# Performance work log

Hardware: AMD Instinct MI355X
Metric: run time of the kernel (lower is better)

Reference implementation:

```python
import jax, jax.numpy as jnp
import numpy as np

B, D_IN, R, D_P, K, D_C, ITERS = 4096, 2048, 7, 128, 25, 16, 3


def _ln(x, g, b, eps=1e-5):
    m = jnp.mean(x, axis=-1, keepdims=True)
    v = jnp.var(x, axis=-1, keepdims=True)
    return (x - m) * jax.lax.rsqrt(v + eps) * g + b


def _squash(x):
    eps = 1e-6
    ns = jnp.sum(x * x, axis=-1, keepdims=True)
    scale = ns / jnp.maximum(1.0 + ns, eps)
    return scale * x / (jnp.sqrt(ns) + eps)


def setup_inputs() -> dict:
    key = jax.random.key(0)
    ks = jax.random.split(key, 8)
    f = lambda k, shp, s=0.02: (jax.random.normal(k, shp) * s).astype(jnp.float32)
    return {
        "z": jax.random.normal(ks[0], (B, D_IN), jnp.float32),
        "W_prim": f(ks[1], (D_IN, R * D_P)),
        "b_prim": jnp.zeros((R * D_P,), jnp.float32),
        "ln_a_g": jnp.ones((D_IN,), jnp.float32),
        "ln_a_b": jnp.zeros((D_IN,), jnp.float32),
        "W_act": f(ks[2], (D_IN, R)),
        "b_act": jnp.zeros((R,), jnp.float32),
        "w_caps": (np.sqrt(K / (D_P * R)).astype(np.float32)
                   * jax.random.normal(ks[3], (R, D_P, K, D_C))).astype(jnp.float32),
        "ln_c_g": jnp.ones((D_C,), jnp.float32),
        "ln_c_b": jnp.zeros((D_C,), jnp.float32),
        "beta_u": f(ks[4], (K,), 1.0),
        "ln_h_g": jnp.ones((R * D_C,), jnp.float32),
        "ln_h_b": jnp.zeros((R * D_C,), jnp.float32),
        "W_h1": f(ks[5], (R * D_C, 4 * R * D_C)),
        "b_h1": jnp.zeros((4 * R * D_C,), jnp.float32),
        "W_h2": f(ks[6], (4 * R * D_C, 1)),
        "b_h2": jnp.zeros((1,), jnp.float32),
    }


def reference(z, W_prim, b_prim, ln_a_g, ln_a_b, W_act, b_act, w_caps,
              ln_c_g, ln_c_b, beta_u, ln_h_g, ln_h_b, W_h1, b_h1, W_h2, b_h2):
    # primary capsules: [B, R, D_P] poses + [B, R] activations
    pose = _squash((z @ W_prim + b_prim).reshape(B, R, D_P))
    act = jnp.clip(jax.nn.sigmoid(_ln(z, ln_a_g, ln_a_b) @ W_act + b_act), 0.0, 1.0)

    # votes: [B, R, K, D_C]
    u = jnp.einsum('brd,rdkh->brkh', pose, w_caps)
    scale = 1.0 / np.sqrt(D_C).astype(np.float32)

    # iterative routing (EM/softmax-agreement style)
    q = jnp.full((B, R, K), 1.0 / K, dtype=z.dtype)
    class_pose = None
    for _ in range(ITERS):
        wts = q * act[:, :, None]                               # [B,R,K]
        class_pose = _ln(jnp.einsum('brk,brkh->bkh', wts, u), ln_c_g, ln_c_b)
        agree = jnp.einsum('bkh,brkh->brk', class_pose, u) * scale
        q = jax.nn.softmax(agree, axis=-1)

    class_act = jax.nn.sigmoid(beta_u[None, :] + jnp.einsum('brk,br->bk', q, act))
    route_class_emb = q[..., None] * u                          # [B,R,K,D_C]

    # concat per-route interaction vectors -> [B, K, R*D_C]
    class_embed = jnp.transpose(route_class_emb, (0, 2, 1, 3)).reshape(B, K, R * D_C)
    h = jax.nn.gelu(_ln(class_embed, ln_h_g, ln_h_b) @ W_h1 + b_h1, approximate=False)
    logits = (h @ W_h2 + b_h2)[..., 0]                          # [B, K]

    return (logits, class_embed, class_pose, class_act, q, pose, act, route_class_emb)
```

## Files before the change

kernel.cpp:

```cpp
#include <hip/hip_runtime.h>
#include <cstddef>

#define BB 4096
#define DIN 2048
#define RR 7
#define DP 128
#define KK 25
#define DC 16
#define NITERS 3
#define RKH (RR*KK*DC)
#define RK  (RR*KK)
#define KH  (KK*DC)
#define HD  (RR*DC)
#define H4  (4*HD)

typedef __attribute__((ext_vector_type(8))) short bf16x8;
typedef __attribute__((ext_vector_type(4))) float f32x4;

__device__ __forceinline__ unsigned pk_bf16(float a, float b) {
    union { float f; unsigned u; } xa, xb;
    xa.f = a; xb.f = b;
    unsigned ua = (xa.u + 0x7FFFu + ((xa.u >> 16) & 1u)) >> 16;
    unsigned ub = (xb.u + 0x7FFFu + ((xb.u >> 16) & 1u)) >> 16;
    return (ua & 0xFFFFu) | (ub << 16);
}

__device__ __forceinline__ float gelu_tanh(float x) {
    float x3 = x * x * x;
    float tt = 0.7978845608f * (x + 0.044715f * x3);
    float e = __expf(2.0f * tt);
    float th = 1.0f - 2.0f / (e + 1.0f);
    return 0.5f * x * (1.0f + th);
}

__global__ __launch_bounds__(256) void transpose_cvt_kernel(
    const float* __restrict__ src, unsigned short* __restrict__ dst, int RS, int CS)
{
    __shared__ float T[64][65];
    int r0 = blockIdx.x * 64, c0 = blockIdx.y * 64;
    size_t bo = (size_t)blockIdx.z * RS * CS;
    src += bo; dst += bo;
    int t = threadIdx.x;
    for (int s = t; s < 64 * 16; s += 256) {
        int row = s >> 4, c4 = s & 15;
        int gr = r0 + row, gc = c0 + c4 * 4;
        float4 v = make_float4(0.f, 0.f, 0.f, 0.f);
        if (gr < RS && gc < CS) v = *(const float4*)(src + (size_t)gr * CS + gc);
        T[row][c4 * 4 + 0] = v.x; T[row][c4 * 4 + 1] = v.y;
        T[row][c4 * 4 + 2] = v.z; T[row][c4 * 4 + 3] = v.w;
    }
    __syncthreads();
    for (int s = t; s < 64 * 16; s += 256) {
        int col = s >> 4, r4 = s & 15;
        int gc = c0 + col, gr = r0 + r4 * 4;
        if (gc < CS && gr + 3 < RS) {
            unsigned lo = pk_bf16(T[r4 * 4 + 0][col], T[r4 * 4 + 1][col]);
            unsigned hi = pk_bf16(T[r4 * 4 + 2][col], T[r4 * 4 + 3][col]);
            *(uint2*)(dst + (size_t)gc * RS + gr) = make_uint2(lo, hi);
        }
    }
}

__global__ __launch_bounds__(256) void w1_frag_kernel(
    const float* __restrict__ W1, unsigned short* __restrict__ W1F)
{
    int d = blockIdx.x * 256 + threadIdx.x;
    int e2 = d & 3;
    int lane = (d >> 2) & 63;
    int fid = d >> 8;
    int j = fid & 3, ks = (fid >> 2) & 3, nc = fid >> 4;
    int col = nc * 64 + j * 16 + (lane & 15);
    int k = ks * 32 + (lane >> 4) * 8 + e2 * 2;
    float a = (k < HD)     ? W1[(size_t)k * H4 + col]       : 0.f;
    float b = (k + 1 < HD) ? W1[(size_t)(k + 1) * H4 + col] : 0.f;
    ((unsigned*)W1F)[d] = pk_bf16(a, b);
}

__global__ __launch_bounds__(256) void act_kernel(
    const float* __restrict__ z, const float* __restrict__ g, const float* __restrict__ bb,
    const float* __restrict__ Wa, const float* __restrict__ ba,
    float* __restrict__ act_out)
{
    int b = blockIdx.x;
    int t = threadIdx.x;
    __shared__ float zs[DIN];
    __shared__ float ws1[4], ws2[4];
    __shared__ float wr[4][RR];
    const float* zr = z + (size_t)b * DIN;
    float s = 0.f, s2 = 0.f;
    for (int i = t; i < DIN; i += 256) {
        float v = zr[i]; zs[i] = v; s += v; s2 += v * v;
    }
    for (int off = 32; off; off >>= 1) { s += __shfl_down(s, off); s2 += __shfl_down(s2, off); }
    int w = t >> 6, lane = t & 63;
    if (lane == 0) { ws1[w] = s; ws2[w] = s2; }
    __syncthreads();
    s  = ws1[0] + ws1[1] + ws1[2] + ws1[3];
    s2 = ws2[0] + ws2[1] + ws2[2] + ws2[3];
    float mean = s * (1.0f / DIN);
    float var  = s2 * (1.0f / DIN) - mean * mean;
    float rstd = rsqrtf(var + 1e-5f);
    float acc[RR];
#pragma unroll
    for (int r = 0; r < RR; ++r) acc[r] = 0.f;
    for (int i = t; i < DIN; i += 256) {
        float y = (zs[i] - mean) * rstd * g[i] + bb[i];
#pragma unroll
        for (int r = 0; r < RR; ++r) acc[r] += y * Wa[i * RR + r];
    }
    for (int off = 32; off; off >>= 1) {
#pragma unroll
        for (int r = 0; r < RR; ++r) acc[r] += __shfl_down(acc[r], off);
    }
    if (lane == 0) {
#pragma unroll
        for (int r = 0; r < RR; ++r) wr[w][r] = acc[r];
    }
    __syncthreads();
    if (t < RR) {
        float v = wr[0][t] + wr[1][t] + wr[2][t] + wr[3][t] + ba[t];
        float sg = 1.0f / (1.0f + expf(-v));
        sg = fminf(fmaxf(sg, 0.0f), 1.0f);
        act_out[(size_t)b * RR + t] = sg;
    }
}

__global__ __launch_bounds__(256) void pose_mfma(
    const float* __restrict__ z, const unsigned short* __restrict__ WpT,
    const float* __restrict__ bp, float* __restrict__ pose_out)
{
    __shared__ __align__(16) unsigned short As[128 * 40];
    __shared__ __align__(16) unsigned short Bs[128 * 40];
    __shared__ float sq[2][128];
    int m0 = blockIdx.x * 128, r = blockIdx.y, t = threadIdx.x;
    int n0 = r * DP;
    int w = t >> 6, l = t & 63;
    int lrow = l & 15, koff = l >> 4;
    int rbase = (w >> 1) * 64, cbase = (w & 1) * 64;
    f32x4 acc[4][4];
#pragma unroll
    for (int i = 0; i < 4; ++i)
#pragma unroll
        for (int j = 0; j < 4; ++j) acc[i][j] = 0.0f;
    for (int kt = 0; kt < DIN; kt += 32) {
#pragma unroll
        for (int q = 0; q < 4; ++q) {
            int s = t + 256 * q;
            int row = s >> 3, k4 = s & 7;
            float4 v = *(const float4*)(z + (size_t)(m0 + row) * DIN + kt + k4 * 4);
            *(uint2*)(As + row * 40 + k4 * 4) = make_uint2(pk_bf16(v.x, v.y), pk_bf16(v.z, v.w));
        }
#pragma unroll
        for (int q = 0; q < 2; ++q) {
            int s = t + 256 * q;
            int col = s >> 2, k8 = s & 3;
            uint4 v = *(const uint4*)(WpT + (size_t)(n0 + col) * DIN + kt + k8 * 8);
            *(uint4*)(Bs + col * 40 + k8 * 8) = v;
        }
        __syncthreads();
        bf16x8 a[4], b[4];
#pragma unroll
        for (int i = 0; i < 4; ++i)
            a[i] = *(const bf16x8*)(As + (rbase + i * 16 + lrow) * 40 + koff * 8);
#pragma unroll
        for (int j = 0; j < 4; ++j)
            b[j] = *(const bf16x8*)(Bs + (cbase + j * 16 + lrow) * 40 + koff * 8);
#pragma unroll
        for (int i = 0; i < 4; ++i)
#pragma unroll
            for (int j = 0; j < 4; ++j)
                acc[i][j] = __builtin_amdgcn_mfma_f32_16x16x32_bf16(a[i], b[j], acc[i][j], 0, 0, 0);
        __syncthreads();
    }
    float bpv[4];
#pragma unroll
    for (int j = 0; j < 4; ++j) bpv[j] = bp[n0 + cbase + j * 16 + lrow];
    float ns_[4][4];
#pragma unroll
    for (int i = 0; i < 4; ++i)
#pragma unroll
        for (int reg = 0; reg < 4; ++reg) {
            float ss = 0.f;
#pragma unroll
            for (int j = 0; j < 4; ++j) {
                float x = acc[i][j][reg] + bpv[j];
                acc[i][j][reg] = x;
                ss += x * x;
            }
            ss += __shfl_xor(ss, 1); ss += __shfl_xor(ss, 2);
            ss += __shfl_xor(ss, 4); ss += __shfl_xor(ss, 8);
            ns_[i][reg] = ss;
        }
    if (lrow == 0) {
#pragma unroll
        for (int i = 0; i < 4; ++i)
#pragma unroll
            for (int reg = 0; reg < 4; ++reg)
                sq[w & 1][rbase + i * 16 + koff * 4 + reg] = ns_[i][reg];
    }
    __syncthreads();
#pragma unroll
    for (int i = 0; i < 4; ++i)
#pragma unroll
        for (int reg = 0; reg < 4; ++reg) {
            int rl = rbase + i * 16 + koff * 4 + reg;
            float ns = sq[0][rl] + sq[1][rl];
            float factor = (ns / fmaxf(1.0f + ns, 1e-6f)) / (sqrtf(ns) + 1e-6f);
            size_t rowbase = ((size_t)(m0 + rl) * RR + r) * DP;
#pragma unroll
            for (int j = 0; j < 4; ++j)
                pose_out[rowbase + cbase + j * 16 + lrow] = acc[i][j][reg] * factor;
        }
}

__global__ __launch_bounds__(256) void votes_mfma(
    const float* __restrict__ pose, const unsigned short* __restrict__ wcT,
    float* __restrict__ u_out)
{
    __shared__ __align__(16) unsigned short As[128 * 152];
    __shared__ __align__(16) unsigned short Bs[80 * 152];
    int m0 = blockIdx.x * 128, r = blockIdx.y, n0 = blockIdx.z * 80;
    int t = threadIdx.x;
    int w = t >> 6, l = t & 63;
    int lrow = l & 15, koff = l >> 4;
    int rbase = w * 32;
#pragma unroll
    for (int q = 0; q < 16; ++q) {
        int s = t + 256 * q;
        int row = s >> 5, k4 = s & 31;
        float4 v = *(const float4*)(pose + ((size_t)(m0 + row) * RR + r) * DP + k4 * 4);
        *(uint2*)(As + row * 152 + k4 * 4) = make_uint2(pk_bf16(v.x, v.y), pk_bf16(v.z, v.w));
    }
    const unsigned short* wr_ = wcT + (size_t)r * KH * DP;
#pragma unroll
    for (int q = 0; q < 5; ++q) {
        int s = t + 256 * q;
        int col = s >> 4, k8 = s & 15;
        uint4 v = *(const uint4*)(wr_ + (size_t)(n0 + col) * DP + k8 * 8);
        *(uint4*)(Bs + col * 152 + k8 * 8) = v;
    }
    __syncthreads();
    f32x4 acc[2][5];
#pragma unroll
    for (int i = 0; i < 2; ++i)
#pragma unroll
        for (int j = 0; j < 5; ++j) acc[i][j] = 0.0f;
#pragma unroll
    for (int ks = 0; ks < 4; ++ks) {
        bf16x8 a[2], b[5];
#pragma unroll
        for (int i = 0; i < 2; ++i)
            a[i] = *(const bf16x8*)(As + (rbase + i * 16 + lrow) * 152 + ks * 32 + koff * 8);
#pragma unroll
        for (int j = 0; j < 5; ++j)
            b[j] = *(const bf16x8*)(Bs + (j * 16 + lrow) * 152 + ks * 32 + koff * 8);
#pragma unroll
        for (int i = 0; i < 2; ++i)
#pragma unroll
            for (int j = 0; j < 5; ++j)
                acc[i][j] = __builtin_amdgcn_mfma_f32_16x16x32_bf16(a[i], b[j], acc[i][j], 0, 0, 0);
    }
#pragma unroll
    for (int i = 0; i < 2; ++i)
#pragma unroll
        for (int reg = 0; reg < 4; ++reg) {
            int row = m0 + rbase + i * 16 + koff * 4 + reg;
            size_t base = ((size_t)row * RR + r) * KH + n0;
#pragma unroll
            for (int j = 0; j < 5; ++j)
                u_out[base + j * 16 + lrow] = acc[i][j][reg];
        }
}

__global__ __launch_bounds__(64) void routing_kernel(
    const float* __restrict__ u_in, const float* __restrict__ act_in,
    const float* __restrict__ lncg, const float* __restrict__ lncb,
    const float* __restrict__ beta_u,
    float* __restrict__ q_out, float* __restrict__ cp_out,
    float* __restrict__ ca_out, float* __restrict__ rce_out,
    float* __restrict__ ce_out)
{
    __shared__ __align__(16) float U[RKH];
    __shared__ float Q[RK];
    __shared__ float CP[KH];
    __shared__ float AG[RK];
    __shared__ float A7[RR];
    int b = blockIdx.x, t = threadIdx.x;
    const float4* u4 = (const float4*)(u_in + (size_t)b * RKH);
    float4* U4 = (float4*)U;
    for (int p = t; p < RKH / 4; p += 64) U4[p] = u4[p];
    if (t < RR) A7[t] = act_in[(size_t)b * RR + t];
    for (int p = t; p < RK; p += 64) Q[p] = 1.0f / KK;
    __syncthreads();
    for (int it = 0; it < NITERS; ++it) {
        for (int p = t; p < KH; p += 64) {
            int k = p / DC;
            float s = 0.f;
#pragma unroll
            for (int r = 0; r < RR; ++r) s += Q[r * KK + k] * A7[r] * U[r * KH + p];
            CP[p] = s;
        }
        __syncthreads();
        if (t < KK) {
            float m = 0.f;
#pragma unroll
            for (int h = 0; h < DC; ++h) m += CP[t * DC + h];
            m *= (1.0f / DC);
            float v = 0.f;
#pragma unroll
            for (int h = 0; h < DC; ++h) { float d = CP[t * DC + h] - m; v += d * d; }
            v *= (1.0f / DC);
            float rstd = rsqrtf(v + 1e-5f);
#pragma unroll
            for (int h = 0; h < DC; ++h)
                CP[t * DC + h] = (CP[t * DC + h] - m) * rstd * lncg[h] + lncb[h];
        }
        __syncthreads();
        for (int p = t; p < RK; p += 64) {
            int r = p / KK, k = p % KK;
            float s = 0.f;
#pragma unroll
            for (int h = 0; h < DC; ++h) s += CP[k * DC + h] * U[r * KH + k * DC + h];
            AG[p] = s * 0.25f;
        }
        __syncthreads();
        if (t < RR) {
            float mx = -1e30f;
            for (int k = 0; k < KK; ++k) mx = fmaxf(mx, AG[t * KK + k]);
            float e[KK], sum = 0.f;
            for (int k = 0; k < KK; ++k) { e[k] = expf(AG[t * KK + k] - mx); sum += e[k]; }
            float inv = 1.0f / sum;
            for (int k = 0; k < KK; ++k) Q[t * KK + k] = e[k] * inv;
        }
        __syncthreads();
    }
    if (t < KK) {
        float s = 0.f;
#pragma unroll
        for (int r = 0; r < RR; ++r) s += Q[r * KK + t] * A7[r];
        ca_out[(size_t)b * KK + t] = 1.0f / (1.0f + expf(-(beta_u[t] + s)));
    }
    for (int p = t; p < RK; p += 64) q_out[(size_t)b * RK + p] = Q[p];
    for (int p = t; p < KH; p += 64) cp_out[(size_t)b * KH + p] = CP[p];
    float4* rce4 = (float4*)(rce_out + (size_t)b * RKH);
    float4* ce4  = (float4*)ce_out;
    for (int p4 = t; p4 < RKH / 4; p4 += 64) {
        int base = p4 * 4;
        int r  = base / KH;
        int k  = (base % KH) / DC;
        int h0 = base % DC;
        float qv = Q[r * KK + k];
        float4 uv = U4[p4];
        float4 rv = make_float4(qv * uv.x, qv * uv.y, qv * uv.z, qv * uv.w);
        rce4[p4] = rv;
        size_t ci = ((size_t)b * RKH + (size_t)k * HD + (size_t)r * DC + h0) >> 2;
        ce4[ci] = rv;
    }
}

__global__ __launch_bounds__(256) void head_mfma(
    const float* __restrict__ ce, const float* __restrict__ g, const float* __restrict__ bb,
    const unsigned short* __restrict__ W1F, const float* __restrict__ b1,
    const float* __restrict__ W2, const float* __restrict__ b2,
    float* __restrict__ logits)
{
    __shared__ __align__(16) unsigned short As[128 * 128];
    __shared__ __align__(16) unsigned short Bs[448 * 128];
    __shared__ float LB1[H4];
    __shared__ float LW2[H4];
    int row0 = blockIdx.x * 128;
    int t = threadIdx.x;
    int w = t >> 6, l = t & 63;
    int lrow = l & 15, koff = l >> 4;

#pragma unroll
    for (int q = 0; q < 28; ++q) {
        int chunk = w * 28 + q;
        __builtin_amdgcn_global_load_lds(
            (const __attribute__((address_space(1))) unsigned int*)(const void*)(W1F + (size_t)chunk * 512 + l * 8),
            (__attribute__((address_space(3))) unsigned int*)(void*)(Bs + chunk * 512),
            16, 0, 0);
    }
    for (int s = t; s < H4; s += 256) { LB1[s] = b1[s]; LW2[s] = W2[s]; }

    {
        int row = t >> 1, half = t & 1;
        const float* rp = ce + (size_t)(row0 + row) * HD + half * 56;
        float4 v[14];
#pragma unroll
        for (int m = 0; m < 14; ++m) v[m] = *(const float4*)(rp + m * 4);
        float s1 = 0.f, s2 = 0.f;
#pragma unroll
        for (int m = 0; m < 14; ++m) {
            s1 += v[m].x + v[m].y + v[m].z + v[m].w;
            s2 += v[m].x * v[m].x + v[m].y * v[m].y + v[m].z * v[m].z + v[m].w * v[m].w;
        }
        s1 += __shfl_xor(s1, 1); s2 += __shfl_xor(s2, 1);
        float mean = s1 * (1.0f / HD);
        float var  = s2 * (1.0f / HD) - mean * mean;
        float rstd = rsqrtf(var + 1e-5f);
        int lr = row & 15, rt = row >> 4;
#pragma unroll
        for (int j = 0; j < 7; ++j) {
            float4 gl0 = *(const float4*)(g  + half * 56 + j * 8);
            float4 gl1 = *(const float4*)(g  + half * 56 + j * 8 + 4);
            float4 bl0 = *(const float4*)(bb + half * 56 + j * 8);
            float4 bl1 = *(const float4*)(bb + half * 56 + j * 8 + 4);
            float4 x0 = v[j * 2], x1 = v[j * 2 + 1];
            float y0 = (x0.x - mean) * rstd * gl0.x + bl0.x;
            float y1 = (x0.y - mean) * rstd * gl0.y + bl0.y;
            float y2 = (x0.z - mean) * rstd * gl0.z + bl0.z;
            float y3 = (x0.w - mean) * rstd * gl0.w + bl0.w;
            float y4 = (x1.x - mean) * rstd * gl1.x + bl1.x;
            float y5 = (x1.y - mean) * rstd * gl1.y + bl1.y;
            float y6 = (x1.z - mean) * rstd * gl1.z + bl1.z;
            float y7 = (x1.w - mean) * rstd * gl1.w + bl1.w;
            int k8 = half * 7 + j;
            int ks = k8 >> 2, ko = k8 & 3;
            unsigned* dst = (unsigned*)(As + (size_t)((rt * 4 + ks) * 64 + ko * 16 + lr) * 8);
            dst[0] = pk_bf16(y0, y1); dst[1] = pk_bf16(y2, y3);
            dst[2] = pk_bf16(y4, y5); dst[3] = pk_bf16(y6, y7);
        }
        if (half) {
            uint4 z4 = make_uint4(0, 0, 0, 0);
            *(uint4*)(As + (size_t)((rt * 4 + 3) * 64 + 2 * 16 + lr) * 8) = z4;
            *(uint4*)(As + (size_t)((rt * 4 + 3) * 64 + 3 * 16 + lr) * 8) = z4;
        }
    }
    __syncthreads();

    bf16x8 af[2][4];
#pragma unroll
    for (int i = 0; i < 2; ++i)
#pragma unroll
        for (int ks = 0; ks < 4; ++ks)
            af[i][ks] = *(const bf16x8*)(As + (size_t)(((w * 2 + i) * 4 + ks) * 64 + l) * 8);

    float logitAcc[2][4];
#pragma unroll
    for (int i = 0; i < 2; ++i)
#pragma unroll
        for (int reg = 0; reg < 4; ++reg) logitAcc[i][reg] = 0.f;

    for (int nc = 0; nc < 7; ++nc) {
        float b1v[4], w2v[4];
#pragma unroll
        for (int j = 0; j < 4; ++j) {
            b1v[j] = LB1[nc * 64 + j * 16 + lrow];
            w2v[j] = LW2[nc * 64 + j * 16 + lrow];
        }
        f32x4 acc[2][4];
#pragma unroll
        for (int i = 0; i < 2; ++i)
#pragma unroll
            for (int j = 0; j < 4; ++j) acc[i][j] = 0.0f;
#pragma unroll
        for (int ks = 0; ks < 4; ++ks) {
            bf16x8 b[4];
#pragma unroll
            for (int j = 0; j < 4; ++j)
                b[j] = *(const bf16x8*)(Bs + (size_t)(((nc * 4 + ks) * 4 + j) * 64 + l) * 8);
#pragma unroll
            for (int i = 0; i < 2; ++i)
#pragma unroll
                for (int j = 0; j < 4; ++j)
                    acc[i][j] = __builtin_amdgcn_mfma_f32_16x16x32_bf16(af[i][ks], b[j], acc[i][j], 0, 0, 0);
        }
#pragma unroll
        for (int i = 0; i < 2; ++i)
#pragma unroll
            for (int reg = 0; reg < 4; ++reg) {
                float sum = 0.f;
#pragma unroll
                for (int j = 0; j < 4; ++j) {
                    float x = acc[i][j][reg] + b1v[j];
                    sum += gelu_tanh(x) * w2v[j];
                }
                logitAcc[i][reg] += sum;
            }
    }
#pragma unroll
    for (int i = 0; i < 2; ++i)
#pragma unroll
        for (int reg = 0; reg < 4; ++reg) {
            float vv = logitAcc[i][reg];
            vv += __shfl_xor(vv, 1); vv += __shfl_xor(vv, 2);
            vv += __shfl_xor(vv, 4); vv += __shfl_xor(vv, 8);
            logitAcc[i][reg] = vv;
        }
    if (lrow == 0) {
        float b2v = b2[0];
#pragma unroll
        for (int i = 0; i < 2; ++i)
#pragma unroll
            for (int reg = 0; reg < 4; ++reg)
                logits[row0 + w * 32 + i * 16 + koff * 4 + reg] = logitAcc[i][reg] + b2v;
    }
}

__global__ __launch_bounds__(256) void pose_kernel(
    const float* __restrict__ z, const float* __restrict__ Wp, const float* __restrict__ bp,
    float* __restrict__ pose_out)
{
    __shared__ __align__(16) float As[64 * 36];
    __shared__ __align__(16) float Bs[32 * 128];
    int m0 = blockIdx.x * 64;
    int r  = blockIdx.y;
    int n0 = r * DP;
    int t  = threadIdx.x;
    int rg = t >> 5;
    int cg = t & 31;
    float acc[8][4] = {};
    for (int kt = 0; kt < DIN; kt += 32) {
#pragma unroll
        for (int q = 0; q < 2; ++q) {
            int s = t * 2 + q;
            int row = s >> 3, k4 = s & 7;
            float4 v = *(const float4*)(z + (size_t)(m0 + row) * DIN + kt + k4 * 4);
            *(float4*)(As + row * 36 + k4 * 4) = v;
        }
#pragma unroll
        for (int q = 0; q < 4; ++q) {
            int s = t + 256 * q;
            int row = s >> 5, c4 = s & 31;
            float4 v = *(const float4*)(Wp + (size_t)(kt + row) * (RR * DP) + n0 + c4 * 4);
            *(float4*)(Bs + row * 128 + c4 * 4) = v;
        }
        __syncthreads();
#pragma unroll
        for (int kk = 0; kk < 32; ++kk) {
            float4 bv = *(const float4*)(Bs + kk * 128 + cg * 4);
#pragma unroll
            for (int j = 0; j < 8; ++j) {
                float a = As[(rg * 8 + j) * 36 + kk];
                acc[j][0] += a * bv.x; acc[j][1] += a * bv.y;
                acc[j][2] += a * bv.z; acc[j][3] += a * bv.w;
            }
        }
        __syncthreads();
    }
    float bi0 = bp[n0 + cg * 4], bi1 = bp[n0 + cg * 4 + 1];
    float bi2 = bp[n0 + cg * 4 + 2], bi3 = bp[n0 + cg * 4 + 3];
#pragma unroll
    for (int j = 0; j < 8; ++j) {
        float x0 = acc[j][0] + bi0, x1 = acc[j][1] + bi1;
        float x2 = acc[j][2] + bi2, x3 = acc[j][3] + bi3;
        float ns = x0 * x0 + x1 * x1 + x2 * x2 + x3 * x3;
        for (int off = 1; off < 32; off <<= 1) ns += __shfl_xor(ns, off);
        float factor = (ns / fmaxf(1.0f + ns, 1e-6f)) / (sqrtf(ns) + 1e-6f);
        int row = m0 + rg * 8 + j;
        float4 o = make_float4(x0 * factor, x1 * factor, x2 * factor, x3 * factor);
        *(float4*)(pose_out + ((size_t)row * RR + r) * DP + cg * 4) = o;
    }
}

__global__ __launch_bounds__(256) void votes_kernel(
    const float* __restrict__ pose, const float* __restrict__ wc,
    float* __restrict__ u_out)
{
    __shared__ float As[64 * 129];
    __shared__ __align__(16) float Bs[64 * 80];
    int m0 = blockIdx.x * 64;
    int r  = blockIdx.y;
    int n0 = blockIdx.z * 80;
    int t  = threadIdx.x;
    const size_t wbase = (size_t)r * DP * KH;
#pragma unroll
    for (int q = 0; q < 8; ++q) {
        int s = t + 256 * q;
        int row = s >> 5, d4 = s & 31;
        float4 v = *(const float4*)(pose + ((size_t)(m0 + row) * RR + r) * DP + d4 * 4);
        As[row * 129 + d4 * 4 + 0] = v.x;
        As[row * 129 + d4 * 4 + 1] = v.y;
        As[row * 129 + d4 * 4 + 2] = v.z;
        As[row * 129 + d4 * 4 + 3] = v.w;
    }
    int m4 = t >> 4, n5 = t & 15;
    float acc[4][5];
#pragma unroll
    for (int i = 0; i < 4; ++i)
#pragma unroll
        for (int j = 0; j < 5; ++j) acc[i][j] = 0.f;
    for (int kt = 0; kt < DP; kt += 64) {
        __syncthreads();
#pragma unroll
        for (int q = 0; q < 5; ++q) {
            int s = t + 256 * q;
            int d = s / 20, c4 = s % 20;
            float4 v = *(const float4*)(wc + wbase + (size_t)(kt + d) * KH + n0 + c4 * 4);
            *(float4*)(Bs + d * 80 + c4 * 4) = v;
        }
        __syncthreads();
#pragma unroll 4
        for (int dd = 0; dd < 64; ++dd) {
            int d = kt + dd;
            float b_[5];
#pragma unroll
            for (int j = 0; j < 5; ++j) b_[j] = Bs[dd * 80 + n5 * 5 + j];
#pragma unroll
            for (int i = 0; i < 4; ++i) {
                float a = As[(m4 * 4 + i) * 129 + d];
#pragma unroll
                for (int j = 0; j < 5; ++j) acc[i][j] += a * b_[j];
            }
        }
    }
#pragma unroll
    for (int i = 0; i < 4; ++i) {
        int row = m0 + m4 * 4 + i;
        size_t base = ((size_t)row * RR + r) * KH + n0 + n5 * 5;
#pragma unroll
        for (int j = 0; j < 5; ++j) u_out[base + j] = acc[i][j];
    }
}

__global__ __launch_bounds__(256) void head_kernel(
    const float* __restrict__ ce, const float* __restrict__ g, const float* __restrict__ bb,
    const float* __restrict__ W1, const float* __restrict__ b1,
    const float* __restrict__ W2, const float* __restrict__ b2,
    float* __restrict__ logits)
{
    __shared__ __align__(16) float Y[64 * HD];
    __shared__ float Wc[HD * 64];
    __shared__ float Lg[64];
    int row0 = blockIdx.x * 64;
    int t = threadIdx.x;
    for (int s = t; s < 64 * HD; s += 256) Y[s] = ce[(size_t)row0 * HD + s];
    __syncthreads();
    if (t < 64) {
        float m = 0.f;
        for (int i = 0; i < HD; ++i) m += Y[t * HD + i];
        m *= (1.0f / HD);
        float v = 0.f;
        for (int i = 0; i < HD; ++i) { float d = Y[t * HD + i] - m; v += d * d; }
        v *= (1.0f / HD);
        float rstd = rsqrtf(v + 1e-5f);
        for (int i = 0; i < HD; ++i) Y[t * HD + i] = (Y[t * HD + i] - m) * rstd * g[i] + bb[i];
    }
    int rg = t >> 4;
    int cg = t & 15;
    float accRow[4] = {0.f, 0.f, 0.f, 0.f};
    for (int c0 = 0; c0 < H4; c0 += 64) {
        __syncthreads();
        for (int s = t; s < HD * 64; s += 256) {
            int i = s >> 6, c = s & 63;
            Wc[i * 64 + c] = W1[(size_t)i * H4 + c0 + c];
        }
        __syncthreads();
        float b1v[4], w2v[4];
#pragma unroll
        for (int c = 0; c < 4; ++c) { b1v[c] = b1[c0 + cg * 4 + c]; w2v[c] = W2[c0 + cg * 4 + c]; }
        float s_[4][4];
#pragma unroll
        for (int rr = 0; rr < 4; ++rr)
#pragma unroll
            for (int c = 0; c < 4; ++c) s_[rr][c] = b1v[c];
        for (int i4 = 0; i4 < HD / 4; ++i4) {
            float4 y4[4];
#pragma unroll
            for (int rr = 0; rr < 4; ++rr)
                y4[rr] = *(const float4*)(Y + (rg * 4 + rr) * HD + i4 * 4);
#pragma unroll
            for (int is = 0; is < 4; ++is) {
                float w_[4];
#pragma unroll
                for (int c = 0; c < 4; ++c) w_[c] = Wc[(i4 * 4 + is) * 64 + cg * 4 + c];
#pragma unroll
                for (int rr = 0; rr < 4; ++rr) {
                    float yv = (is == 0) ? y4[rr].x : (is == 1) ? y4[rr].y : (is == 2) ? y4[rr].z : y4[rr].w;
#pragma unroll
                    for (int c = 0; c < 4; ++c) s_[rr][c] += yv * w_[c];
                }
            }
        }
#pragma unroll
        for (int rr = 0; rr < 4; ++rr) {
#pragma unroll
            for (int c = 0; c < 4; ++c) {
                float x = s_[rr][c];
                float ge = 0.5f * x * (1.0f + erff(x * 0.70710678118654752440f));
                accRow[rr] += ge * w2v[c];
            }
        }
    }
#pragma unroll
    for (int rr = 0; rr < 4; ++rr) {
        float v = accRow[rr];
        v += __shfl_xor(v, 1); v += __shfl_xor(v, 2);
        v += __shfl_xor(v, 4); v += __shfl_xor(v, 8);
        if (cg == 0) Lg[rg * 4 + rr] = v;
    }
    __syncthreads();
    if (t < 64) logits[row0 + t] = Lg[t] + b2[0];
}

extern "C" void kernel_launch(void* const* d_in, const int* in_sizes, int n_in,
                              void* d_out, int out_size, void* d_ws, size_t ws_size,
                              hipStream_t stream) {
    const float* z    = (const float*)d_in[0];
    const float* Wp   = (const float*)d_in[1];
    const float* bp   = (const float*)d_in[2];
    const float* lnag = (const float*)d_in[3];
    const float* lnab = (const float*)d_in[4];
    const float* Wa   = (const float*)d_in[5];
    const float* ba   = (const float*)d_in[6];
    const float* wc   = (const float*)d_in[7];
    const float* lncg = (const float*)d_in[8];
    const float* lncb = (const float*)d_in[9];
    const float* beta = (const float*)d_in[10];
    const float* lnhg = (const float*)d_in[11];
    const float* lnhb = (const float*)d_in[12];
    const float* W1   = (const float*)d_in[13];
    const float* b1   = (const float*)d_in[14];
    const float* W2   = (const float*)d_in[15];
    const float* b2   = (const float*)d_in[16];

    float* out = (float*)d_out;
    float* o_logits = out;
    float* o_ce   = o_logits + (size_t)BB * KK;
    float* o_cp   = o_ce   + (size_t)BB * KK * HD;
    float* o_ca   = o_cp   + (size_t)BB * KK * DC;
    float* o_q    = o_ca   + (size_t)BB * KK;
    float* o_pose = o_q    + (size_t)BB * RK;
    float* o_act  = o_pose + (size_t)BB * RR * DP;
    float* o_rce  = o_act  + (size_t)BB * RR;

    const size_t WPT_ELE = (size_t)(RR * DP) * DIN;
    const size_t W1F_ELE = (size_t)H4 * 128;
    const size_t WCT_ELE = (size_t)RR * KH * DP;
    const size_t WS_NEED = (WPT_ELE + W1F_ELE + WCT_ELE) * sizeof(unsigned short);
    unsigned short* WpT = (unsigned short*)d_ws;
    unsigned short* W1F = WpT + WPT_ELE;
    unsigned short* wcT = W1F + W1F_ELE;

    hipLaunchKernelGGL(act_kernel, dim3(BB), dim3(256), 0, stream,
                       z, lnag, lnab, Wa, ba, o_act);

    if (ws_size >= WS_NEED) {
        hipLaunchKernelGGL(transpose_cvt_kernel, dim3(DIN / 64, (RR * DP) / 64, 1), dim3(256), 0, stream,
                           Wp, WpT, DIN, RR * DP);
        hipLaunchKernelGGL(w1_frag_kernel, dim3(112), dim3(256), 0, stream,
                           W1, W1F);
        hipLaunchKernelGGL(transpose_cvt_kernel, dim3(2, 7, RR), dim3(256), 0, stream,
                           wc, wcT, DP, KH);
        hipLaunchKernelGGL(pose_mfma, dim3(BB / 128, RR), dim3(256), 0, stream,
                           z, WpT, bp, o_pose);
        hipLaunchKernelGGL(votes_mfma, dim3(BB / 128, RR, 5), dim3(256), 0, stream,
                           o_pose, wcT, o_rce);
        hipLaunchKernelGGL(routing_kernel, dim3(BB), dim3(64), 0, stream,
                           o_rce, o_act, lncg, lncb, beta, o_q, o_cp, o_ca, o_rce, o_ce);
        hipLaunchKernelGGL(head_mfma, dim3(BB * KK / 128), dim3(256), 0, stream,
                           o_ce, lnhg, lnhb, W1F, b1, W2, b2, o_logits);
    } else {
        hipLaunchKernelGGL(pose_kernel, dim3(BB / 64, RR), dim3(256), 0, stream,
                           z, Wp, bp, o_pose);
        hipLaunchKernelGGL(votes_kernel, dim3(BB / 64, RR, 5), dim3(256), 0, stream,
                           o_pose, wc, o_rce);
        hipLaunchKernelGGL(routing_kernel, dim3(BB), dim3(64), 0, stream,
                           o_rce, o_act, lncg, lncb, beta, o_q, o_cp, o_ca, o_rce, o_ce);
        hipLaunchKernelGGL(head_kernel, dim3(BB * KK / 64), dim3(256), 0, stream,
                           o_ce, lnhg, lnhb, W1, b1, W2, b2, o_logits);
    }
}
```

Baseline: 382.6 us.

## Make head kernel persistent with 512 threads, prefetch next tile, cheaper GELU

The head MLP kernel becomes persistent: 256 blocks of 512 threads loop over the 800 row tiles. Each block loads the bf16 W1 fragments into LDS once instead of once per tile. While the MFMAs for the current tile run, half the threads prefetch the next tile's class-embedding rows into registers. Each wave now computes 16 rows instead of 32, and the tanh-form GELU is rewritten as a sigmoid form using a fast reciprocal. The cost is more synchronisation per tile, less per-wave MFMA reuse of each B fragment, and a slightly different approximation of GELU.

```diff
diff --git a/kernel.cpp b/kernel.cpp
--- a/kernel.cpp
+++ b/kernel.cpp
@@ -13,6 +13,7 @@
 #define KH  (KK*DC)
 #define HD  (RR*DC)
 #define H4  (4*HD)
+#define HEAD_TILES (BB*KK/128)
 
 typedef __attribute__((ext_vector_type(8))) short bf16x8;
 typedef __attribute__((ext_vector_type(4))) float f32x4;
@@ -31,6 +32,13 @@
     float e = __expf(2.0f * tt);
     float th = 1.0f - 2.0f / (e + 1.0f);
     return 0.5f * x * (1.0f + th);
+}
+
+__device__ __forceinline__ float gelu_fast(float x) {
+    float u = x * __builtin_fmaf(x * x, 0.07135655f, 1.5957691f);
+    u = fmaxf(u, -30.0f);
+    float e = __expf(-u);
+    return x * __builtin_amdgcn_rcpf(1.0f + e);
 }
 
 __global__ __launch_bounds__(256) void transpose_cvt_kernel(
@@ -358,7 +366,7 @@
     }
 }
 
-__global__ __launch_bounds__(256) void head_mfma(
+__global__ __launch_bounds__(512) void head_mfma(
     const float* __restrict__ ce, const float* __restrict__ g, const float* __restrict__ bb,
     const unsigned short* __restrict__ W1F, const float* __restrict__ b1,
     const float* __restrict__ W2, const float* __restrict__ b2,
@@ -368,133 +376,133 @@
     __shared__ __align__(16) unsigned short Bs[448 * 128];
     __shared__ float LB1[H4];
     __shared__ float LW2[H4];
-    int row0 = blockIdx.x * 128;
     int t = threadIdx.x;
     int w = t >> 6, l = t & 63;
     int lrow = l & 15, koff = l >> 4;
 
 #pragma unroll
-    for (int q = 0; q < 28; ++q) {
-        int chunk = w * 28 + q;
+    for (int q = 0; q < 14; ++q) {
+        int chunk = w * 14 + q;
         __builtin_amdgcn_global_load_lds(
             (const __attribute__((address_space(1))) unsigned int*)(const void*)(W1F + (size_t)chunk * 512 + l * 8),
             (__attribute__((address_space(3))) unsigned int*)(void*)(Bs + chunk * 512),
             16, 0, 0);
     }
-    for (int s = t; s < H4; s += 256) { LB1[s] = b1[s]; LW2[s] = W2[s]; }
-
-    {
-        int row = t >> 1, half = t & 1;
-        const float* rp = ce + (size_t)(row0 + row) * HD + half * 56;
-        float4 v[14];
+    if (t >= 256) {
+        for (int s = t - 256; s < H4; s += 256) { LB1[s] = b1[s]; LW2[s] = W2[s]; }
+    }
+    float b2v = b2[0];
+
+    int row = t >> 1, half = t & 1;
+    int lr = row & 15, rt = row >> 4;
+
+    float4 v[14];
+    int tile = blockIdx.x;
+    if (t < 256 && tile < HEAD_TILES) {
+        const float* rp = ce + (size_t)(tile * 128 + row) * HD + half * 56;
 #pragma unroll
         for (int m = 0; m < 14; ++m) v[m] = *(const float4*)(rp + m * 4);
-        float s1 = 0.f, s2 = 0.f;
-#pragma unroll
-        for (int m = 0; m < 14; ++m) {
-            s1 += v[m].x + v[m].y + v[m].z + v[m].w;
-            s2 += v[m].x * v[m].x + v[m].y * v[m].y + v[m].z * v[m].z + v[m].w * v[m].w;
-        }
-        s1 += __shfl_xor(s1, 1); s2 += __shfl_xor(s2, 1);
-        float mean = s1 * (1.0f / HD);
-        float var  = s2 * (1.0f / HD) - mean * mean;
-        float rstd = rsqrtf(var + 1e-5f);
-        int lr = row & 15, rt = row >> 4;
-#pragma unroll
-        for (int j = 0; j < 7; ++j) {
-            float4 gl0 = *(const float4*)(g  + half * 56 + j * 8);
-            float4 gl1 = *(const float4*)(g  + half * 56 + j * 8 + 4);
-            float4 bl0 = *(const float4*)(bb + half * 56 + j * 8);
-            float4 bl1 = *(const float4*)(bb + half * 56 + j * 8 + 4);
-            float4 x0 = v[j * 2], x1 = v[j * 2 + 1];
-            float y0 = (x0.x - mean) * rstd * gl0.x + bl0.x;
-            float y1 = (x0.y - mean) * rstd * gl0.y + bl0.y;
-            float y2 = (x0.z - mean) * rstd * gl0.z + bl0.z;
-            float y3 = (x0.w - mean) * rstd * gl0.w + bl0.w;
-            float y4 = (x1.x - mean) * rstd * gl1.x + bl1.x;
-            float y5 = (x1.y - mean) * rstd * gl1.y + bl1.y;
-            float y6 = (x1.z - mean) * rstd * gl1.z + bl1.z;
-            float y7 = (x1.w - mean) * rstd * gl1.w + bl1.w;
-            int k8 = half * 7 + j;
-            int ks = k8 >> 2, ko = k8 & 3;
-            unsigned* dst = (unsigned*)(As + (size_t)((rt * 4 + ks) * 64 + ko * 16 + lr) * 8);
-            dst[0] = pk_bf16(y0, y1); dst[1] = pk_bf16(y2, y3);
-            dst[2] = pk_bf16(y4, y5); dst[3] = pk_bf16(y6, y7);
-        }
-        if (half) {
-            uint4 z4 = make_uint4(0, 0, 0, 0);
-            *(uint4*)(As + (size_t)((rt * 4 + 3) * 64 + 2 * 16 + lr) * 8) = z4;
-            *(uint4*)(As + (size_t)((rt * 4 + 3) * 64 + 3 * 16 + lr) * 8) = z4;
-        }
-    }
-    __syncthreads();
-
-    bf16x8 af[2][4];
-#pragma unroll
-    for (int i = 0; i < 2; ++i)
+    }
+
+    bool first = true;
+    for (; tile < HEAD_TILES; tile += 256) {
+        if (!first) __syncthreads();
+        first = false;
+
+        if (t < 256) {
+            float s1 = 0.f, s2 = 0.f;
+#pragma unroll
+            for (int m = 0; m < 14; ++m) {
+                s1 += v[m].x + v[m].y + v[m].z + v[m].w;
+                s2 += v[m].x * v[m].x + v[m].y * v[m].y + v[m].z * v[m].z + v[m].w * v[m].w;
+            }
+            s1 += __shfl_xor(s1, 1); s2 += __shfl_xor(s2, 1);
+            float mean = s1 * (1.0f / HD);
+            float var  = s2 * (1.0f / HD) - mean * mean;
+            float rstd = rsqrtf(var + 1e-5f);
+#pragma unroll
+            for (int j = 0; j < 7; ++j) {
+                float4 gl0 = *(const float4*)(g  + half * 56 + j * 8);
+                float4 gl1 = *(const float4*)(g  + half * 56 + j * 8 + 4);
+                float4 bl0 = *(const float4*)(bb + half * 56 + j * 8);
+                float4 bl1 = *(const float4*)(bb + half * 56 + j * 8 + 4);
+                float4 x0 = v[j * 2], x1 = v[j * 2 + 1];
+                float y0 = (x0.x - mean) * rstd * gl0.x + bl0.x;
+                float y1 = (x0.y - mean) * rstd * gl0.y + bl0.y;
+                float y2 = (x0.z - mean) * rstd * gl0.z + bl0.z;
+                float y3 = (x0.w - mean) * rstd * gl0.w + bl0.w;
+                float y4 = (x1.x - mean) * rstd * gl1.x + bl1.x;
+                float y5 = (x1.y - mean) * rstd * gl1.y + bl1.y;
+                float y6 = (x1.z - mean) * rstd * gl1.z + bl1.z;
+                float y7 = (x1.w - mean) * rstd * gl1.w + bl1.w;
+                int k8 = half * 7 + j;
+                int ks = k8 >> 2, ko = k8 & 3;
+                unsigned* dst = (unsigned*)(As + (size_t)((rt * 4 + ks) * 64 + ko * 16 + lr) * 8);
+                dst[0] = pk_bf16(y0, y1); dst[1] = pk_bf16(y2, y3);
+                dst[2] = pk_bf16(y4, y5); dst[3] = pk_bf16(y6, y7);
+            }
+            if (half) {
+                uint4 z4 = make_uint4(0, 0, 0, 0);
+                *(uint4*)(As + (size_t)((rt * 4 + 3) * 64 + 2 * 16 + lr) * 8) = z4;
+                *(uint4*)(As + (size_t)((rt * 4 + 3) * 64 + 3 * 16 + lr) * 8) = z4;
+            }
+        }
+        __syncthreads();
+
+        bf16x8 af[4];
 #pragma unroll
         for (int ks = 0; ks < 4; ++ks)
-            af[i][ks] = *(const bf16x8*)(As + (size_t)(((w * 2 + i) * 4 + ks) * 64 + l) * 8);
-
-    float logitAcc[2][4];
-#pragma unroll
-    for (int i = 0; i < 2; ++i)
-#pragma unroll
-        for (int reg = 0; reg < 4; ++reg) logitAcc[i][reg] = 0.f;
-
-    for (int nc = 0; nc < 7; ++nc) {
-        float b1v[4], w2v[4];
-#pragma unroll
-        for (int j = 0; j < 4; ++j) {
-            b1v[j] = LB1[nc * 64 + j * 16 + lrow];
-            w2v[j] = LW2[nc * 64 + j * 16 + lrow];
-        }
-        f32x4 acc[2][4];
-#pragma unroll
-        for (int i = 0; i < 2; ++i)
-#pragma unroll
-            for (int j = 0; j < 4; ++j) acc[i][j] = 0.0f;
-#pragma unroll
-        for (int ks = 0; ks < 4; ++ks) {
-            bf16x8 b[4];
-#pragma unroll
-            for (int j = 0; j < 4; ++j)
-                b[j] = *(const bf16x8*)(Bs + (size_t)(((nc * 4 + ks) * 4 + j) * 64 + l) * 8);
-#pragma unroll
-            for (int i = 0; i < 2; ++i)
+            af[ks] = *(const bf16x8*)(As + (size_t)((w * 4 + ks) * 64 + l) * 8);
+
+        if (t < 256 && tile + 256 < HEAD_TILES) {
+            const float* rp = ce + (size_t)((tile + 256) * 128 + row) * HD + half * 56;
+#pragma unroll
+            for (int m = 0; m < 14; ++m) v[m] = *(const float4*)(rp + m * 4);
+        }
+
+        float logitAcc[4];
+#pragma unroll
+        for (int reg = 0; reg < 4; ++reg) logitAcc[reg] = 0.f;
+
+        for (int nc = 0; nc < 7; ++nc) {
+            float b1v[4], w2v[4];
+#pragma unroll
+            for (int j = 0; j < 4; ++j) {
+                b1v[j] = LB1[nc * 64 + j * 16 + lrow];
+                w2v[j] = LW2[nc * 64 + j * 16 + lrow];
+            }
+            f32x4 acc[4];
+#pragma unroll
+            for (int j = 0; j < 4; ++j) acc[j] = 0.0f;
+#pragma unroll
+            for (int ks = 0; ks < 4; ++ks) {
+                bf16x8 bfr[4];
 #pragma unroll
                 for (int j = 0; j < 4; ++j)
-                    acc[i][j] = __builtin_amdgcn_mfma_f32_16x16x32_bf16(af[i][ks], b[j], acc[i][j], 0, 0, 0);
-        }
-#pragma unroll
-        for (int i = 0; i < 2; ++i)
+                    bfr[j] = *(const bf16x8*)(Bs + (size_t)(((nc * 4 + ks) * 4 + j) * 64 + l) * 8);
+#pragma unroll
+                for (int j = 0; j < 4; ++j)
+                    acc[j] = __builtin_amdgcn_mfma_f32_16x16x32_bf16(af[ks], bfr[j], acc[j], 0, 0, 0);
+            }
 #pragma unroll
             for (int reg = 0; reg < 4; ++reg) {
                 float sum = 0.f;
 #pragma unroll
                 for (int j = 0; j < 4; ++j) {
-                    float x = acc[i][j][reg] + b1v[j];
-                    sum += gelu_tanh(x) * w2v[j];
+                    float x = acc[j][reg] + b1v[j];
+                    sum += gelu_fast(x) * w2v[j];
                 }
-                logitAcc[i][reg] += sum;
-            }
-    }
-#pragma unroll
-    for (int i = 0; i < 2; ++i)
+                logitAcc[reg] += sum;
+            }
+        }
 #pragma unroll
         for (int reg = 0; reg < 4; ++reg) {
-            float vv = logitAcc[i][reg];
+            float vv = logitAcc[reg];
             vv += __shfl_xor(vv, 1); vv += __shfl_xor(vv, 2);
             vv += __shfl_xor(vv, 4); vv += __shfl_xor(vv, 8);
-            logitAcc[i][reg] = vv;
-        }
-    if (lrow == 0) {
-        float b2v = b2[0];
-#pragma unroll
-        for (int i = 0; i < 2; ++i)
-#pragma unroll
-            for (int reg = 0; reg < 4; ++reg)
-                logits[row0 + w * 32 + i * 16 + koff * 4 + reg] = logitAcc[i][reg] + b2v;
+            if (lrow == 0)
+                logits[(size_t)tile * 128 + w * 16 + koff * 4 + reg] = vv + b2v;
+        }
     }
 }
 
@@ -749,7 +757,7 @@
                            o_pose, wcT, o_rce);
         hipLaunchKernelGGL(routing_kernel, dim3(BB), dim3(64), 0, stream,
                            o_rce, o_act, lncg, lncb, beta, o_q, o_cp, o_ca, o_rce, o_ce);
-        hipLaunchKernelGGL(head_mfma, dim3(BB * KK / 128), dim3(256), 0, stream,
+        hipLaunchKernelGGL(head_mfma, dim3(256), dim3(512), 0, stream,
                            o_ce, lnhg, lnhb, W1F, b1, W2, b2, o_logits);
     } else {
         hipLaunchKernelGGL(pose_kernel, dim3(BB / 64, RR), dim3(256), 0, stream,
```

Measured after the change: 351.9 us. 8.0% less time.
